# Performance work log

Hardware: AMD Instinct MI355X
Metric: run time of the kernel (lower is better)

The kernel has to match this reference:

```python
import jax, jax.numpy as jnp
import numpy as np

N = 50000
E = 800000
IN_CH = 128
HIDDEN = 32
HEADS = 4
OUT_CH = 64
NEG_SLOPE = 0.2


def setup_inputs() -> dict:
    key = jax.random.key(0)
    ks = jax.random.split(key, 12)
    x = jax.random.normal(ks[0], (N, IN_CH), dtype=jnp.float32)
    edge_index = jax.random.randint(ks[1], (2, E), 0, N, dtype=jnp.int64)
    # layer 1: GATConv(IN_CH, HIDDEN, heads=4, concat=True)
    s1 = 1.0 / np.sqrt(IN_CH)
    W1 = jax.random.normal(ks[2], (IN_CH, HEADS * HIDDEN), dtype=jnp.float32) * s1
    att_src1 = jax.random.normal(ks[3], (HEADS, HIDDEN), dtype=jnp.float32) * 0.1
    att_dst1 = jax.random.normal(ks[4], (HEADS, HIDDEN), dtype=jnp.float32) * 0.1
    b1 = jnp.zeros((HEADS * HIDDEN,), dtype=jnp.float32)
    # layer 2: GATConv(HEADS*HIDDEN, OUT_CH, heads=1, concat=False)
    s2 = 1.0 / np.sqrt(HEADS * HIDDEN)
    W2 = jax.random.normal(ks[5], (HEADS * HIDDEN, OUT_CH), dtype=jnp.float32) * s2
    att_src2 = jax.random.normal(ks[6], (1, OUT_CH), dtype=jnp.float32) * 0.1
    att_dst2 = jax.random.normal(ks[7], (1, OUT_CH), dtype=jnp.float32) * 0.1
    b2 = jnp.zeros((OUT_CH,), dtype=jnp.float32)
    return {"x": x, "edge_index": edge_index, "W1": W1, "att_src1": att_src1,
            "att_dst1": att_dst1, "b1": b1, "W2": W2, "att_src2": att_src2,
            "att_dst2": att_dst2, "b2": b2}


def gat_conv(x, src, dst, W, a_src, a_dst, bias, heads, out_ch, concat):
    n = x.shape[0]
    h = (x @ W).reshape(n, heads, out_ch)               # [N, H, C]
    alpha_s = jnp.sum(h * a_src[None], axis=-1)          # [N, H]
    alpha_d = jnp.sum(h * a_dst[None], axis=-1)          # [N, H]
    e = alpha_s[src] + alpha_d[dst]                      # [E, H]
    e = jnp.where(e > 0, e, NEG_SLOPE * e)               # leaky_relu(0.2)
    # segment softmax over incoming edges of each dst node
    e_max = jax.ops.segment_max(e, dst, num_segments=n)
    e_max = jnp.where(jnp.isfinite(e_max), e_max, 0.0)
    ex = jnp.exp(e - e_max[dst])
    denom = jax.ops.segment_sum(ex, dst, num_segments=n)
    alpha = ex / (denom[dst] + 1e-16)                    # [E, H]
    msg = h[src] * alpha[:, :, None]                     # [E, H, C]
    out = jax.ops.segment_sum(msg, dst, num_segments=n)  # [N, H, C]
    if concat:
        out = out.reshape(n, heads * out_ch)
    else:
        out = out.mean(axis=1)
    return out + bias


def reference(x, edge_index, W1, att_src1, att_dst1, b1, W2, att_src2, att_dst2, b2):
    n = x.shape[0]
    loop = jnp.arange(n, dtype=edge_index.dtype)
    src = jnp.concatenate([edge_index[0], loop])  # add self-loops (PyG default)
    dst = jnp.concatenate([edge_index[1], loop])
    h = gat_conv(x, src, dst, W1, att_src1, att_dst1, b1, HEADS, HIDDEN, True)
    h = jax.nn.elu(h)
    return gat_conv(h, src, dst, W2, att_src2, att_dst2, b2, 1, OUT_CH, False)
```

## Files before the change

### kernel.cpp

```cpp
#include <hip/hip_runtime.h>

#define NN    50000
#define NE    800000
#define NET   850000
#define NBUCK ((NN + 255) / 256)
#define MAXB  8192
#define BINB  256

typedef __fp16 half2_t __attribute__((ext_vector_type(2)));
typedef _Float16 half8 __attribute__((ext_vector_type(8)));
typedef float floatx4 __attribute__((ext_vector_type(4)));

__device__ __forceinline__ float lrelu(float v) { return fmaxf(v, 0.2f * v); }
__device__ __forceinline__ unsigned pk16(float a, float b) {
    half2_t h = __builtin_amdgcn_cvt_pkrtz(a, b);
    return __builtin_bit_cast(unsigned, h);
}
__device__ __forceinline__ float2 unpk16(unsigned u) {
    half2_t h = __builtin_bit_cast(half2_t, u);
    return make_float2((float)h.x, (float)h.y);
}

__global__ __launch_bounds__(256) void gemm1_mfma_kernel(
    const float* __restrict__ x, const _Float16* __restrict__ w1t,
    const float* __restrict__ att_s, const float* __restrict__ att_d,
    _Float16* __restrict__ h1h, float* __restrict__ as, float* __restrict__ ad)
{
    __shared__ _Float16 lw[128 * 128];
    __shared__ _Float16 hs[64 * 128];
    const int t    = threadIdx.x;
    const int lane = t & 63;
    const int m    = lane & 15;
    const int q    = lane >> 4;
    const int wv   = t >> 6;
    const int gr0  = blockIdx.x * 64;
    const int rbase = gr0 + wv * 16;

    const int rme = rbase + m;
    const int rc  = rme < NN ? rme : NN - 1;
    const float* ap = x + (size_t)rc * 128 + q * 8;

    float4 f0[4], f1[4];
#pragma unroll
    for (int ks = 0; ks < 4; ks++) {
        f0[ks] = *(const float4*)(ap + ks * 32);
        f1[ks] = *(const float4*)(ap + ks * 32 + 4);
    }

    {
        const int kb = t & 15;
        const int n0 = t >> 4;
#pragma unroll
        for (int it = 0; it < 8; it++) {
            const int n = n0 + it * 16;
            const uint4 v = *(const uint4*)(w1t + n * 128 + kb * 8);
            *(uint4*)((char*)lw + n * 256 + ((kb * 16) ^ ((n & 7) << 4))) = v;
        }
    }
    __syncthreads();

    floatx4 acc[8];
#pragma unroll
    for (int nt = 0; nt < 8; nt++) acc[nt] = (floatx4){0.f, 0.f, 0.f, 0.f};

    const int swz = (m & 7) << 4;
#pragma unroll
    for (int ks = 0; ks < 4; ks++) {
        const uint4 au = make_uint4(pk16(f0[ks].x, f0[ks].y), pk16(f0[ks].z, f0[ks].w),
                                    pk16(f1[ks].x, f1[ks].y), pk16(f1[ks].z, f1[ks].w));
        const half8 a = __builtin_bit_cast(half8, au);
#pragma unroll
        for (int nt = 0; nt < 8; nt++) {
            const int n = nt * 16 + m;
            const half8 b = *(const half8*)((const char*)lw + n * 256 +
                                            ((ks * 64 + q * 16) ^ swz));
            acc[nt] = __builtin_amdgcn_mfma_f32_16x16x32_f16(a, b, acc[nt], 0, 0, 0);
        }
    }

    const int lrow0 = wv * 16 + q * 4;
#pragma unroll
    for (int nt = 0; nt < 8; nt++)
#pragma unroll
        for (int r = 0; r < 4; r++)
            hs[(lrow0 + r) * 128 + nt * 16 + m] = (_Float16)acc[nt][r];
    __syncthreads();

#pragma unroll
    for (int i = t; i < 1024; i += 256) {
        const int row = i >> 4;
        if (gr0 + row < NN)
            ((half8*)h1h)[(size_t)(gr0 + row) * 16 + (i & 15)] = ((const half8*)hs)[i];
    }

    const int arow = t >> 2, hd = t & 3;
    const int grow = gr0 + arow;
    float ps = 0.f, pd = 0.f;
    const half8*  hp8 = (const half8*)(hs + arow * 128 + hd * 32);
    const float4* s4  = (const float4*)(att_s + hd * 32);
    const float4* d4  = (const float4*)(att_d + hd * 32);
#pragma unroll
    for (int cc = 0; cc < 4; cc++) {
        const half8 hv = hp8[cc];
        const float4 a = s4[cc * 2], b = s4[cc * 2 + 1];
        const float4 c = d4[cc * 2], e = d4[cc * 2 + 1];
        ps += (float)hv[0]*a.x + (float)hv[1]*a.y + (float)hv[2]*a.z + (float)hv[3]*a.w
            + (float)hv[4]*b.x + (float)hv[5]*b.y + (float)hv[6]*b.z + (float)hv[7]*b.w;
        pd += (float)hv[0]*c.x + (float)hv[1]*c.y + (float)hv[2]*c.z + (float)hv[3]*c.w
            + (float)hv[4]*e.x + (float)hv[5]*e.y + (float)hv[6]*e.z + (float)hv[7]*e.w;
    }
    if (grow < NN) {
        as[grow * 4 + hd] = ps;
        ad[grow * 4 + hd] = pd;
    }
}

__global__ __launch_bounds__(256) void gemm2_mfma_kernel(
    const _Float16* __restrict__ ah, const _Float16* __restrict__ w2t,
    const float* __restrict__ att_s, const float* __restrict__ att_d,
    _Float16* __restrict__ h2h, float* __restrict__ as, float* __restrict__ ad)
{
    __shared__ _Float16 lw[64 * 128];
    __shared__ _Float16 hs[64 * 64];
    const int t    = threadIdx.x;
    const int lane = t & 63;
    const int m    = lane & 15;
    const int q    = lane >> 4;
    const int wv   = t >> 6;
    const int gr0  = blockIdx.x * 64;
    const int rbase = gr0 + wv * 16;

    const int rme = rbase + m;
    const int rc  = rme < NN ? rme : NN - 1;
    const _Float16* ap = ah + (size_t)rc * 128 + q * 8;

    half8 av[4];
#pragma unroll
    for (int ks = 0; ks < 4; ks++) av[ks] = *(const half8*)(ap + ks * 32);

    {
        const int kb = t & 15;
        const int n0 = t >> 4;
#pragma unroll
        for (int it = 0; it < 4; it++) {
            const int n = n0 + it * 16;
            const uint4 v = *(const uint4*)(w2t + n * 128 + kb * 8);
            *(uint4*)((char*)lw + n * 256 + ((kb * 16) ^ ((n & 7) << 4))) = v;
        }
    }
    __syncthreads();

    floatx4 acc[4];
#pragma unroll
    for (int nt = 0; nt < 4; nt++) acc[nt] = (floatx4){0.f, 0.f, 0.f, 0.f};

    const int swz = (m & 7) << 4;
#pragma unroll
    for (int ks = 0; ks < 4; ks++) {
#pragma unroll
        for (int nt = 0; nt < 4; nt++) {
            const int n = nt * 16 + m;
            const half8 b = *(const half8*)((const char*)lw + n * 256 +
                                            ((ks * 64 + q * 16) ^ swz));
            acc[nt] = __builtin_amdgcn_mfma_f32_16x16x32_f16(av[ks], b, acc[nt], 0, 0, 0);
        }
    }

    const int lrow0 = wv * 16 + q * 4;
#pragma unroll
    for (int nt = 0; nt < 4; nt++)
#pragma unroll
        for (int r = 0; r < 4; r++)
            hs[(lrow0 + r) * 64 + nt * 16 + m] = (_Float16)acc[nt][r];
    __syncthreads();

#pragma unroll
    for (int i = t; i < 512; i += 256) {
        const int row = i >> 3;
        if (gr0 + row < NN)
            ((half8*)h2h)[(size_t)(gr0 + row) * 8 + (i & 7)] = ((const half8*)hs)[i];
    }

    const int arow = t >> 2, sg = t & 3;
    const int grow = gr0 + arow;
    float ps = 0.f, pd = 0.f;
    const half8*  hp8 = (const half8*)(hs + arow * 64 + sg * 16);
    const float4* s4  = (const float4*)(att_s + sg * 16);
    const float4* d4  = (const float4*)(att_d + sg * 16);
#pragma unroll
    for (int cc = 0; cc < 2; cc++) {
        const half8 hv = hp8[cc];
        const float4 a = s4[cc * 2], b = s4[cc * 2 + 1];
        const float4 c = d4[cc * 2], e = d4[cc * 2 + 1];
        ps += (float)hv[0]*a.x + (float)hv[1]*a.y + (float)hv[2]*a.z + (float)hv[3]*a.w
            + (float)hv[4]*b.x + (float)hv[5]*b.y + (float)hv[6]*b.z + (float)hv[7]*b.w;
        pd += (float)hv[0]*c.x + (float)hv[1]*c.y + (float)hv[2]*c.z + (float)hv[3]*c.w
            + (float)hv[4]*e.x + (float)hv[5]*e.y + (float)hv[6]*e.z + (float)hv[7]*e.w;
    }
    ps += __shfl_down(ps, 2);  pd += __shfl_down(pd, 2);
    ps += __shfl_down(ps, 1);  pd += __shfl_down(pd, 1);
    if (sg == 0 && grow < NN) { as[grow] = ps; ad[grow] = pd; }
}

__global__ __launch_bounds__(1024) void bin_kernel(const int* __restrict__ ei,
                                                   const float* __restrict__ W1,
                                                   const float* __restrict__ W2,
                                                   _Float16* __restrict__ w1t,
                                                   _Float16* __restrict__ w2t,
                                                   int* __restrict__ bcnt,
                                                   unsigned* __restrict__ pairs)
{
    if (blockIdx.x < 24) {
        const int idx = blockIdx.x * 1024 + threadIdx.x;
        if (idx < 16384) {
            const int k = idx >> 7, n = idx & 127;
            w1t[n * 128 + k] = (_Float16)W1[idx];
        } else {
            const int j = idx - 16384;
            const int k = j >> 6, n = j & 63;
            w2t[n * 128 + k] = (_Float16)W2[j];
        }
    }

    __shared__ int hist[NBUCK], base[NBUCK], cur[NBUCK];
    const int t = threadIdx.x;
    if (t < NBUCK) { hist[t] = 0; cur[t] = 0; }
    __syncthreads();

    for (int e = blockIdx.x * 1024 + t; e < NET; e += BINB * 1024) {
        const int d = (e < NE) ? ei[NE + e] : (e - NE);
        atomicAdd(&hist[d >> 8], 1);
    }
    __syncthreads();
    if (t < NBUCK && hist[t]) base[t] = atomicAdd(&bcnt[t * 16], hist[t]);
    __syncthreads();
    for (int e = blockIdx.x * 1024 + t; e < NET; e += BINB * 1024) {
        int s, d;
        if (e < NE) { s = ei[e]; d = ei[NE + e]; } else { s = d = e - NE; }
        const int bk = d >> 8;
        const int r = atomicAdd(&cur[bk], 1);
        pairs[(size_t)bk * MAXB + base[bk] + r] =
            (unsigned)s | ((unsigned)(d & 255) << 16);
    }
}

__global__ __launch_bounds__(1024) void bsort_kernel(
    const int* __restrict__ bcnt, const unsigned* __restrict__ pairs,
    int* __restrict__ row_beg, int* __restrict__ row_end,
    int* __restrict__ col)
{
    __shared__ int hist[256], cur[256], sh[256];
    __shared__ int outl[MAXB];
    const int b = blockIdx.x, t = threadIdx.x;
    const int m = bcnt[b * 16];
    const int gbase = b * MAXB;
    if (t < 256) hist[t] = 0;
    __syncthreads();
    for (int i = t; i < m; i += 1024)
        atomicAdd(&hist[pairs[gbase + i] >> 16], 1);
    __syncthreads();
    if (t < 256) sh[t] = hist[t];
    __syncthreads();
#pragma unroll
    for (int off = 1; off < 256; off <<= 1) {
        int u = (t < 256 && t >= off) ? sh[t - off] : 0;
        __syncthreads();
        if (t < 256) sh[t] += u;
        __syncthreads();
    }
    if (t < 256) {
        const int ex = sh[t] - hist[t];
        cur[t] = ex;
        const int node = (b << 8) + t;
        if (node < NN) {
            row_beg[node] = gbase + ex;
            row_end[node] = gbase + ex + hist[t];
        }
    }
    __syncthreads();
    for (int i = t; i < m; i += 1024) {
        const unsigned p = pairs[gbase + i];
        const int r = atomicAdd(&cur[p >> 16], 1);
        outl[r] = (int)(p & 0xFFFFu);
    }
    __syncthreads();
    for (int i = t; i < m; i += 1024) col[gbase + i] = outl[i];
}

__global__ __launch_bounds__(256) void agg1_fused_kernel(
    const int* __restrict__ row_beg, const int* __restrict__ row_end,
    const int* __restrict__ col, const unsigned* __restrict__ hh,
    const float* __restrict__ as1, const float* __restrict__ ad1,
    const float* __restrict__ b1, unsigned* __restrict__ acth)
{
    __shared__ float wbuf[4][64 * 4];
    const int wv   = threadIdx.x >> 6;
    const int d    = __builtin_amdgcn_readfirstlane((blockIdx.x * 256 + threadIdx.x) >> 6);
    const int lane = threadIdx.x & 63;
    const int head = lane >> 4;
    const int beg = row_beg[d], end = row_end[d];
    const float4 ad4 = ((const float4*)ad1)[d];
    float* wb = wbuf[wv];

    float acc0 = 0.f, acc1 = 0.f, den = 0.f;

    for (int jb = beg; jb < end; jb += 64) {
        const int cnt = min(64, end - jb);
        {
            const int sl = col[jb + min(lane, cnt - 1)];
            const float4 a = ((const float4*)as1)[sl];
            float4 w4;
            w4.x = __expf(lrelu(a.x + ad4.x));
            w4.y = __expf(lrelu(a.y + ad4.y));
            w4.z = __expf(lrelu(a.z + ad4.z));
            w4.w = __expf(lrelu(a.w + ad4.w));
            ((float4*)wb)[lane] = w4;
        }
        __asm__ volatile("s_waitcnt lgkmcnt(0)" ::: "memory");

        int k = 0;
        for (; k + 16 <= cnt; k += 16) {
            float    w[16];
            unsigned g[16];
#pragma unroll
            for (int u = 0; u < 16; u++) {
                const int s = col[jb + k + u];
                w[u] = wb[(k + u) * 4 + head];
                g[u] = hh[s * 64 + lane];
            }
#pragma unroll
            for (int u = 0; u < 16; u++) {
                const float2 g2 = unpk16(g[u]);
                den  += w[u];
                acc0 += w[u] * g2.x;
                acc1 += w[u] * g2.y;
            }
        }
        for (; k + 4 <= cnt; k += 4) {
            float    w[4];
            unsigned g[4];
#pragma unroll
            for (int u = 0; u < 4; u++) {
                const int s = col[jb + k + u];
                w[u] = wb[(k + u) * 4 + head];
                g[u] = hh[s * 64 + lane];
            }
#pragma unroll
            for (int u = 0; u < 4; u++) {
                const float2 g2 = unpk16(g[u]);
                den  += w[u];
                acc0 += w[u] * g2.x;
                acc1 += w[u] * g2.y;
            }
        }
        for (; k < cnt; k++) {
            const float w = wb[k * 4 + head];
            const float2 g2 = unpk16(hh[col[jb + k] * 64 + lane]);
            den  += w;
            acc0 += w * g2.x;
            acc1 += w * g2.y;
        }
        __asm__ volatile("" ::: "memory");
    }
    const float2 bb  = ((const float2*)b1)[lane];
    const float  inv = 1.f / (den + 1e-16f);
    float v0 = acc0 * inv + bb.x;
    float v1 = acc1 * inv + bb.y;
    v0 = v0 > 0.f ? v0 : (__expf(v0) - 1.f);
    v1 = v1 > 0.f ? v1 : (__expf(v1) - 1.f);
    acth[d * 64 + lane] = pk16(v0, v1);
}

__global__ __launch_bounds__(256) void agg2_fused_kernel(
    const int* __restrict__ row_beg, const int* __restrict__ row_end,
    const int* __restrict__ col, const _Float16* __restrict__ h,
    const float* __restrict__ as2, const float* __restrict__ ad2,
    const float* __restrict__ b2, float* __restrict__ out)
{
    __shared__ float wbuf[4][64];
    const int wv   = threadIdx.x >> 6;
    const int d    = __builtin_amdgcn_readfirstlane((blockIdx.x * 256 + threadIdx.x) >> 6);
    const int lane = threadIdx.x & 63;
    const int beg = row_beg[d], end = row_end[d];
    const float add = ad2[d];
    float* wb = wbuf[wv];

    float acc = 0.f, den = 0.f;

    for (int jb = beg; jb < end; jb += 64) {
        const int cnt = min(64, end - jb);
        {
            const int sl = col[jb + min(lane, cnt - 1)];
            wb[lane] = __expf(lrelu(as2[sl] + add));
        }
        __asm__ volatile("s_waitcnt lgkmcnt(0)" ::: "memory");

        int k = 0;
        for (; k + 16 <= cnt; k += 16) {
            float w[16], g[16];
#pragma unroll
            for (int u = 0; u < 16; u++) {
                const int s = col[jb + k + u];
                w[u] = wb[k + u];
                g[u] = (float)h[s * 64 + lane];
            }
#pragma unroll
            for (int u = 0; u < 16; u++) {
                den += w[u];
                acc += w[u] * g[u];
            }
        }
        for (; k + 4 <= cnt; k += 4) {
            float w[4], g[4];
#pragma unroll
            for (int u = 0; u < 4; u++) {
                const int s = col[jb + k + u];
                w[u] = wb[k + u];
                g[u] = (float)h[s * 64 + lane];
            }
#pragma unroll
            for (int u = 0; u < 4; u++) {
                den += w[u];
                acc += w[u] * g[u];
            }
        }
        for (; k < cnt; k++) {
            const float w = wb[k];
            den += w;
            acc += w * (float)h[col[jb + k] * 64 + lane];
        }
        __asm__ volatile("" ::: "memory");
    }
    out[d * 64 + lane] = acc / (den + 1e-16f) + b2[lane];
}

extern "C" void kernel_launch(void* const* d_in, const int* in_sizes, int n_in,
                              void* d_out, int out_size, void* d_ws, size_t ws_size,
                              hipStream_t stream)
{
    const float* x    = (const float*)d_in[0];
    const int*   ei   = (const int*)  d_in[1];
    const float* W1   = (const float*)d_in[2];
    const float* at_s1= (const float*)d_in[3];
    const float* at_d1= (const float*)d_in[4];
    const float* b1   = (const float*)d_in[5];
    const float* W2   = (const float*)d_in[6];
    const float* at_s2= (const float*)d_in[7];
    const float* at_d2= (const float*)d_in[8];
    const float* b2   = (const float*)d_in[9];
    float*       out  = (float*)d_out;

    const size_t NPAD = (size_t)NBUCK * MAXB;

    float* fw   = (float*)d_ws;
    float* as1  = fw;
    float* ad1  = as1  + NN * 4;
    float* as2  = ad1  + NN * 4;
    float* ad2  = as2  + NN;
    _Float16* h1h   = (_Float16*)(ad2 + NN);
    _Float16* act1h = h1h  + (size_t)NN * 128;
    _Float16* h2h   = act1h+ (size_t)NN * 128;
    _Float16* w1t   = h2h  + (size_t)NN * 64;
    _Float16* w2t   = w1t  + 16384;
    int*   row_beg = (int*)(w2t + 8192);
    int*   row_end = row_beg + NN;
    int*   col     = row_end + NN;
    int*   bcnt    = col + NPAD;
    unsigned* pairs = (unsigned*)(bcnt + 4096);

    hipMemsetAsync(bcnt, 0, 4096 * sizeof(int), stream);

    const int gemm_grid = (NN + 63) / 64;
    const int node_wave_grid = NN / 4;

    bin_kernel  <<<BINB, 1024, 0, stream>>>(ei, W1, W2, w1t, w2t, bcnt, pairs);
    bsort_kernel<<<NBUCK, 1024, 0, stream>>>(bcnt, pairs, row_beg, row_end, col);

    gemm1_mfma_kernel<<<gemm_grid, 256, 0, stream>>>(x, w1t, at_s1, at_d1, h1h, as1, ad1);
    agg1_fused_kernel<<<node_wave_grid, 256, 0, stream>>>(row_beg, row_end, col,
                        (const unsigned*)h1h, as1, ad1, b1, (unsigned*)act1h);

    gemm2_mfma_kernel<<<gemm_grid, 256, 0, stream>>>(act1h, w2t, at_s2, at_d2, h2h, as2, ad2);
    agg2_fused_kernel<<<node_wave_grid, 256, 0, stream>>>(row_beg, row_end, col,
                        h2h, as2, ad2, b2, out);
}
```

Before: 186.1 us.

## Split agg2 edges across wave halves with packed half2 loads; enlarge agg blocks

```diff
diff --git a/kernel.cpp b/kernel.cpp
--- a/kernel.cpp
+++ b/kernel.cpp
@@ -6,6 +6,7 @@
 #define NBUCK ((NN + 255) / 256)
 #define MAXB  8192
 #define BINB  256
+#define AGGB  3125
 
 typedef __fp16 half2_t __attribute__((ext_vector_type(2)));
 typedef _Float16 half8 __attribute__((ext_vector_type(8)));
@@ -287,15 +288,15 @@
     for (int i = t; i < m; i += 1024) col[gbase + i] = outl[i];
 }
 
-__global__ __launch_bounds__(256) void agg1_fused_kernel(
+__global__ __launch_bounds__(1024) void agg1_fused_kernel(
     const int* __restrict__ row_beg, const int* __restrict__ row_end,
     const int* __restrict__ col, const unsigned* __restrict__ hh,
     const float* __restrict__ as1, const float* __restrict__ ad1,
     const float* __restrict__ b1, unsigned* __restrict__ acth)
 {
-    __shared__ float wbuf[4][64 * 4];
+    __shared__ float wbuf[16][64 * 4];
     const int wv   = threadIdx.x >> 6;
-    const int d    = __builtin_amdgcn_readfirstlane((blockIdx.x * 256 + threadIdx.x) >> 6);
+    const int d    = __builtin_amdgcn_readfirstlane(blockIdx.x * 16 + wv);
     const int lane = threadIdx.x & 63;
     const int head = lane >> 4;
     const int beg = row_beg[d], end = row_end[d];
@@ -371,21 +372,24 @@
     acth[d * 64 + lane] = pk16(v0, v1);
 }
 
-__global__ __launch_bounds__(256) void agg2_fused_kernel(
+__global__ __launch_bounds__(1024) void agg2_fused_kernel(
     const int* __restrict__ row_beg, const int* __restrict__ row_end,
     const int* __restrict__ col, const _Float16* __restrict__ h,
     const float* __restrict__ as2, const float* __restrict__ ad2,
     const float* __restrict__ b2, float* __restrict__ out)
 {
-    __shared__ float wbuf[4][64];
+    __shared__ float wbuf[16][64];
     const int wv   = threadIdx.x >> 6;
-    const int d    = __builtin_amdgcn_readfirstlane((blockIdx.x * 256 + threadIdx.x) >> 6);
+    const int d    = __builtin_amdgcn_readfirstlane(blockIdx.x * 16 + wv);
     const int lane = threadIdx.x & 63;
+    const int half = lane >> 5;
+    const int c    = lane & 31;
     const int beg = row_beg[d], end = row_end[d];
     const float add = ad2[d];
     float* wb = wbuf[wv];
-
-    float acc = 0.f, den = 0.f;
+    const unsigned* __restrict__ h2 = (const unsigned*)h;
+
+    float acc0 = 0.f, acc1 = 0.f, den = 0.f;
 
     for (int jb = beg; jb < end; jb += 64) {
         const int cnt = min(64, end - jb);
@@ -397,41 +401,47 @@
 
         int k = 0;
         for (; k + 16 <= cnt; k += 16) {
-            float w[16], g[16];
-#pragma unroll
-            for (int u = 0; u < 16; u++) {
-                const int s = col[jb + k + u];
-                w[u] = wb[k + u];
-                g[u] = (float)h[s * 64 + lane];
-            }
-#pragma unroll
-            for (int u = 0; u < 16; u++) {
-                den += w[u];
-                acc += w[u] * g[u];
-            }
-        }
-        for (; k + 4 <= cnt; k += 4) {
-            float w[4], g[4];
-#pragma unroll
-            for (int u = 0; u < 4; u++) {
-                const int s = col[jb + k + u];
-                w[u] = wb[k + u];
-                g[u] = (float)h[s * 64 + lane];
-            }
-#pragma unroll
-            for (int u = 0; u < 4; u++) {
-                den += w[u];
-                acc += w[u] * g[u];
-            }
-        }
-        for (; k < cnt; k++) {
-            const float w = wb[k];
-            den += w;
-            acc += w * (float)h[col[jb + k] * 64 + lane];
+            float    w[8];
+            unsigned g[8];
+#pragma unroll
+            for (int u = 0; u < 8; u++) {
+                const int e = jb + k + 2 * u + half;
+                const int s = col[e];
+                w[u] = wb[k + 2 * u + half];
+                g[u] = h2[(size_t)s * 32 + c];
+            }
+#pragma unroll
+            for (int u = 0; u < 8; u++) {
+                const float2 g2 = unpk16(g[u]);
+                den  += w[u];
+                acc0 += w[u] * g2.x;
+                acc1 += w[u] * g2.y;
+            }
+        }
+        for (; k < cnt; k += 2) {
+            const int  e   = k + half;
+            const bool ok  = e < cnt;
+            const int  s   = col[jb + (ok ? e : cnt - 1)];
+            const float w  = ok ? wb[e] : 0.f;
+            const float2 g2 = unpk16(h2[(size_t)s * 32 + c]);
+            den  += w;
+            acc0 += w * g2.x;
+            acc1 += w * g2.y;
         }
         __asm__ volatile("" ::: "memory");
     }
-    out[d * 64 + lane] = acc / (den + 1e-16f) + b2[lane];
+    acc0 += __shfl_xor(acc0, 32);
+    acc1 += __shfl_xor(acc1, 32);
+    den  += __shfl_xor(den, 32);
+
+    if (half == 0) {
+        const float inv = 1.f / (den + 1e-16f);
+        const float2 bb = ((const float2*)b2)[c];
+        float2 o;
+        o.x = acc0 * inv + bb.x;
+        o.y = acc1 * inv + bb.y;
+        ((float2*)out)[(size_t)d * 32 + c] = o;
+    }
 }
 
 extern "C" void kernel_launch(void* const* d_in, const int* in_sizes, int n_in,
@@ -471,16 +481,15 @@
     hipMemsetAsync(bcnt, 0, 4096 * sizeof(int), stream);
 
     const int gemm_grid = (NN + 63) / 64;
-    const int node_wave_grid = NN / 4;
 
     bin_kernel  <<<BINB, 1024, 0, stream>>>(ei, W1, W2, w1t, w2t, bcnt, pairs);
     bsort_kernel<<<NBUCK, 1024, 0, stream>>>(bcnt, pairs, row_beg, row_end, col);
 
     gemm1_mfma_kernel<<<gemm_grid, 256, 0, stream>>>(x, w1t, at_s1, at_d1, h1h, as1, ad1);
-    agg1_fused_kernel<<<node_wave_grid, 256, 0, stream>>>(row_beg, row_end, col,
+    agg1_fused_kernel<<<AGGB, 1024, 0, stream>>>(row_beg, row_end, col,
                         (const unsigned*)h1h, as1, ad1, b1, (unsigned*)act1h);
 
     gemm2_mfma_kernel<<<gemm_grid, 256, 0, stream>>>(act1h, w2t, at_s2, at_d2, h2h, as2, ad2);
-    agg2_fused_kernel<<<node_wave_grid, 256, 0, stream>>>(row_beg, row_end, col,
+    agg2_fused_kernel<<<AGGB, 1024, 0, stream>>>(row_beg, row_end, col,
                         h2h, as2, ad2, b2, out);
 }
```

New measurement: 206.5 us. +10.9%, slower.
